# Performance work log

Measured on AMD Instinct MI355X. Metric: run time of the kernel, lower is better.

The kernel has to match this reference:

```python
import jax, jax.numpy as jnp
import numpy as np

B, L, HID = 1, 4096, 2048
H, P, N, CH, K = 64, 64, 128, 256, 4
INTER = H * P              # 4096 = num_heads * head_dim
CONV_DIM = INTER + 2 * N   # 4352
OUT_IN = 2 * (INTER + N) + H  # 8512, d_mlp == 0
DT_MIN, DT_MAX, EPS = 0.0, 100.0, 1e-5


def setup_inputs() -> dict:
    key = jax.random.key(0)
    ks = jax.random.split(key, 6)
    hidden_states = jax.random.normal(ks[0], (B, L, HID), jnp.float32)
    W_in = jax.random.normal(ks[1], (HID, OUT_IN), jnp.float32) * 0.02
    conv_w = jax.random.normal(ks[2], (K, CONV_DIM), jnp.float32) * 0.1
    conv_b = jnp.zeros((CONV_DIM,), jnp.float32)
    # dt_bias = softplus^{-1}(dt), dt ~ LogUniform[1e-3, 1e-1] (matches init_dt_bias)
    u = jax.random.uniform(ks[3], (H,))
    dt = jnp.exp(u * (jnp.log(0.1) - jnp.log(0.001)) + jnp.log(0.001))
    dt_bias = dt + jnp.log(-jnp.expm1(-dt))
    A_log = jnp.log(jax.random.uniform(ks[4], (H,), minval=1.0, maxval=16.0))
    D = jnp.ones((H,), jnp.float32)
    norm_weight = jnp.ones((INTER,), jnp.float32)
    W_out = jax.random.normal(ks[5], (INTER, HID), jnp.float32) * 0.02
    return dict(hidden_states=hidden_states, W_in=W_in, conv_w=conv_w, conv_b=conv_b,
                dt_bias=dt_bias, A_log=A_log, D=D, norm_weight=norm_weight, W_out=W_out)


def reference(hidden_states, W_in, conv_w, conv_b, dt_bias, A_log, D, norm_weight, W_out):
    Bsz, Ls, _ = hidden_states.shape
    nc = Ls // CH  # number of chunks

    zxbcdt = hidden_states @ W_in  # (b, l, 2*inter + 2*N + H); d_mlp = 0
    z, xBC, dt = jnp.split(zxbcdt, [INTER, 2 * INTER + 2 * N], axis=-1)

    # causal depthwise conv1d (left-pad K-1) + silu
    xp = jnp.pad(xBC, ((0, 0), (K - 1, 0), (0, 0)))
    xBC = sum(xp[:, k:k + Ls, :] * conv_w[k] for k in range(K)) + conv_b
    xBC = jax.nn.silu(xBC)
    x, Bt, Ct = jnp.split(xBC, [INTER, INTER + N], axis=-1)
    x = x.reshape(Bsz, Ls, H, P)

    dt = jnp.clip(jax.nn.softplus(dt + dt_bias), DT_MIN, DT_MAX)  # (b, l, h)
    A = -jnp.exp(A_log)  # (h,), negative

    # ---- chunked SSD (structured state-space duality) ----
    xc = x.reshape(Bsz, nc, CH, H, P)
    Bc = Bt.reshape(Bsz, nc, CH, N)   # shared across heads
    Cc = Ct.reshape(Bsz, nc, CH, N)
    dtc = dt.reshape(Bsz, nc, CH, H)
    xdt = xc * dtc[..., None]                     # discretized input
    dA = jnp.transpose(dtc * A, (0, 3, 1, 2))     # (b, h, c, l)
    A_cs = jnp.cumsum(dA, axis=-1)                # (b, h, c, l)

    # intra-chunk causal decay matrix L[i,j] = exp(sum_{j<k<=i} dA[k])
    seg = A_cs[..., :, None] - A_cs[..., None, :]
    tri = jnp.tril(jnp.ones((CH, CH), bool))
    Lmat = jnp.where(tri, jnp.exp(seg), 0.0)      # (b, h, c, l, s)
    Y_diag = jnp.einsum('bcln,bcsn,bhcls,bcshp->bclhp', Cc, Bc, Lmat, xdt)

    # per-chunk end states
    decay_states = jnp.exp(A_cs[..., -1:] - A_cs)  # (b, h, c, l)
    states = jnp.einsum('bcln,bhcl,bclhp->bchpn', Bc, decay_states, xdt)

    # inter-chunk recurrence via decay matrix over chunks (initial state = 0)
    chunk_end = A_cs[..., -1]                                     # (b, h, c)
    pad_cs = jnp.pad(jnp.cumsum(chunk_end, axis=-1), ((0, 0), (0, 0), (1, 0)))
    segc = pad_cs[..., :, None] - pad_cs[..., None, :]            # (b, h, c+1, c+1)
    tric = jnp.tril(jnp.ones((nc + 1, nc + 1), bool))
    decay_chunk = jnp.where(tric, jnp.exp(segc), 0.0)
    init = jnp.zeros((Bsz, 1, H, P, N), states.dtype)
    states = jnp.concatenate([init, states], axis=1)              # (b, c+1, h, p, n)
    new_states = jnp.einsum('bhzc,bchpn->bzhpn', decay_chunk, states)
    states_in = new_states[:, :-1]                                # state entering each chunk

    state_decay = jnp.exp(A_cs)  # (b, h, c, l)
    Y_off = jnp.einsum('bcln,bchpn,bhcl->bclhp', Cc, states_in, state_decay)

    y = (Y_diag + Y_off).reshape(Bsz, Ls, H, P)
    y = y + x * D[None, None, :, None]            # skip connection
    y = y.reshape(Bsz, Ls, INTER)

    # gated RMSNorm: rmsnorm(y * silu(z)) * weight  (fp32 internally)
    yf = y.astype(jnp.float32) * jax.nn.silu(z.astype(jnp.float32))
    var = jnp.mean(yf * yf, axis=-1, keepdims=True)
    yf = yf * jax.lax.rsqrt(var + EPS) * norm_weight
    y = yf.astype(hidden_states.dtype)

    return y @ W_out
```

## Files before the change

kernel.cpp:

```cpp
#include <hip/hip_runtime.h>
#include <hip/hip_bf16.h>
#include <math.h>

typedef __bf16 bf16x8 __attribute__((ext_vector_type(8)));
typedef float f32x4 __attribute__((ext_vector_type(4)));

#define GLOBAL_LOAD_LDS16(gptr, lptr) \
  __builtin_amdgcn_global_load_lds((const __attribute__((address_space(1))) void*)(gptr), \
                                   (__attribute__((address_space(3))) void*)(lptr), 16, 0, 0)

__device__ __forceinline__ void tile_map(int bid, int nbx, int nby, int& bx, int& by) {
  int nwg = nbx * nby;
  int q = nwg >> 3, r = nwg & 7;
  int xcd = bid & 7, orig = bid >> 3;
  int wgid = (xcd < r ? xcd * (q + 1) : r * (q + 1) + (xcd - r) * q) + orig;
  int per = nbx << 3;
  int grp = wgid / per;
  int rem = wgid - grp * per;
  int g0 = grp << 3;
  int gm = nby - g0; if (gm > 8) gm = 8;
  by = g0 + rem % gm;
  bx = rem / gm;
}

template<int MODE>
__global__ __launch_bounds__(256, 3)
void gemm_kernel(const __bf16* __restrict__ A, const __bf16* __restrict__ BT,
                 int M, int N, int K, int Ktot,
                 __bf16* __restrict__ out0, float* __restrict__ out2,
                 __bf16* yio, float* __restrict__ ssum,
                 const float* __restrict__ nwp)
{
  __shared__ __align__(16) __bf16 As[128 * 64];
  __shared__ __align__(16) __bf16 Bs[128 * 64];
  const int tid  = threadIdx.x;
  const int wave = tid >> 6, lane = tid & 63;
  const int quad = lane >> 4, l16 = lane & 15;
  int bx, by;
  tile_map(blockIdx.y * gridDim.x + blockIdx.x, gridDim.x, gridDim.y, bx, by);
  const int mBase = by * 128;
  const int nBase = bx * 128;
  const int wm = (wave & 1) * 64;
  const int wn = (wave >> 1) * 64;
  const int kb = (MODE == 3) ? blockIdx.z : 0;
  const int kStart = kb * K, kEnd = kb * K + K;

  f32x4 acc[4][4] = {};

  for (int k0 = kStart; k0 < kEnd; k0 += 64) {
    __syncthreads();
    for (int rd = 0; rd < 4; ++rd) {
      int p = rd * 256 + tid;
      int row = p >> 3;
      int lc  = (p & 7) ^ (row & 7);
      const __bf16* gpA = A + (size_t)(mBase + row) * Ktot + k0 + lc * 8;
      GLOBAL_LOAD_LDS16(gpA, As + rd * 2048 + wave * 512);
      int gr = nBase + row; if (gr >= N) gr = N - 1;
      const __bf16* gpB = BT + (size_t)gr * Ktot + k0 + lc * 8;
      GLOBAL_LOAD_LDS16(gpB, Bs + rd * 2048 + wave * 512);
    }
    __syncthreads();
#pragma unroll
    for (int ks = 0; ks < 2; ++ks) {
      bf16x8 af[4], bfr[4];
#pragma unroll
      for (int i = 0; i < 4; ++i) {
        int r = wm + i * 16 + l16;
        af[i]  = *(const bf16x8*)(As + (r << 6) + (((ks * 4 + quad) ^ (r & 7)) << 3));
        int rb = wn + i * 16 + l16;
        bfr[i] = *(const bf16x8*)(Bs + (rb << 6) + (((ks * 4 + quad) ^ (rb & 7)) << 3));
      }
#pragma unroll
      for (int i = 0; i < 4; ++i)
#pragma unroll
        for (int j = 0; j < 4; ++j)
          acc[i][j] = __builtin_amdgcn_mfma_f32_16x16x32_bf16(af[i], bfr[j], acc[i][j], 0, 0, 0);
    }
  }

  if (MODE == 2) {
    for (int i = 0; i < 4; ++i)
      for (int r = 0; r < 4; ++r) {
        int row = mBase + wm + i * 16 + quad * 4 + r;
        float sq = 0.f;
        for (int j = 0; j < 4; ++j) {
          int col = nBase + wn + j * 16 + l16;
          float v = acc[i][j][r];
          size_t idx = (size_t)row * 4096 + col;
          float y0 = (float)yio[idx];
          float zg = v / (1.f + expf(-v));
          float yf = y0 * zg;
          yio[idx] = (__bf16)(yf * nwp[col]);
          sq += yf * yf;
        }
        for (int m = 1; m < 16; m <<= 1) sq += __shfl_xor(sq, m, 64);
        if (l16 == 0) atomicAdd(&ssum[row], sq);
      }
  } else if (MODE == 3) {
    float rs[4][4];
    for (int i = 0; i < 4; ++i)
      for (int r = 0; r < 4; ++r) {
        int row = mBase + wm + i * 16 + quad * 4 + r;
        rs[i][r] = rsqrtf(ssum[row] / 4096.f + 1e-5f);
      }
    for (int i = 0; i < 4; ++i) {
      int rowl = wm + i * 16 + quad * 4;
      for (int j = 0; j < 4; ++j) {
        int col = nBase + wn + j * 16 + l16;
        for (int r = 0; r < 4; ++r) {
          int row = mBase + rowl + r;
          float o = acc[i][j][r] * rs[i][r];
          o = (o == o && fabsf(o) < 1e30f) ? o : 0.f;
          out2[(size_t)row * N + col] = o;
        }
      }
    }
  } else {
    for (int i = 0; i < 4; ++i) {
      int rowl = wm + i * 16 + quad * 4;
      for (int j = 0; j < 4; ++j) {
        int col = nBase + wn + j * 16 + l16;
        for (int r = 0; r < 4; ++r) {
          float v = acc[i][j][r];
          int row = mBase + rowl + r;
          if (col < 4352)       out0[(size_t)row * 4352 + col]        = (__bf16)v;
          else if (col < 4416)  out2[(size_t)row * 64 + (col - 4352)] = v;
        }
      }
    }
  }
}

__global__ __launch_bounds__(256)
void cast_kernel(const float* __restrict__ in, __bf16* __restrict__ out)
{
  size_t g = ((size_t)blockIdx.x * 256 + threadIdx.x) * 8;
  f32x4 a = *(const f32x4*)(in + g);
  f32x4 b = *(const f32x4*)(in + g + 4);
  bf16x8 v;
  for (int j = 0; j < 4; ++j) { v[j] = (__bf16)a[j]; v[4 + j] = (__bf16)b[j]; }
  *(bf16x8*)(out + g) = v;
}

__global__ __launch_bounds__(256)
void transpose_kernel(const float* __restrict__ in, __bf16* __restrict__ out,
                      int R, int C, int col0)
{
  __shared__ __bf16 tile[64][72];
  const int tid = threadIdx.x;
  const int r0 = blockIdx.y * 64, c0 = blockIdx.x * 64;
  const int tr = tid >> 3, tc = (tid & 7) * 8;
  for (int hh = 0; hh < 2; ++hh) {
    const float* gp = in + (size_t)(r0 + tr + hh * 32) * C + col0 + c0 + tc;
    f32x4 a = *(const f32x4*)gp;
    f32x4 b = *(const f32x4*)(gp + 4);
    for (int j = 0; j < 4; ++j) {
      tile[tr + hh * 32][tc + j]     = (__bf16)a[j];
      tile[tr + hh * 32][tc + 4 + j] = (__bf16)b[j];
    }
  }
  __syncthreads();
  for (int hh = 0; hh < 2; ++hh) {
    __bf16* op = out + (size_t)(c0 + tr + hh * 32) * R + r0 + tc;
    bf16x8 o;
    for (int j = 0; j < 8; ++j) o[j] = tile[tc + j][tr + hh * 32];
    *(bf16x8*)op = o;
  }
}

__global__ __launch_bounds__(256)
void conv_silu_kernel(const __bf16* __restrict__ xBCraw, const float* __restrict__ conv_w,
                      const float* __restrict__ conv_b,
                      __bf16* __restrict__ xconv, __bf16* __restrict__ Bmat,
                      __bf16* __restrict__ Cmat, __bf16* __restrict__ BTr)
{
  int g = blockIdx.x * 256 + threadIdx.x;
  int t = g / 544;
  int c = (g % 544) * 8;
  float acc[8];
  {
    f32x4 b0 = *(const f32x4*)(conv_b + c);
    f32x4 b1 = *(const f32x4*)(conv_b + c + 4);
    for (int j = 0; j < 4; ++j) { acc[j] = b0[j]; acc[4 + j] = b1[j]; }
  }
  for (int k = 0; k < 4; ++k) {
    int ts = t + k - 3;
    if (ts >= 0) {
      bf16x8 xv = *(const bf16x8*)(xBCraw + (size_t)ts * 4352 + c);
      f32x4 w0 = *(const f32x4*)(conv_w + (size_t)k * 4352 + c);
      f32x4 w1 = *(const f32x4*)(conv_w + (size_t)k * 4352 + c + 4);
      for (int j = 0; j < 4; ++j) {
        acc[j]     += (float)xv[j]     * w0[j];
        acc[4 + j] += (float)xv[4 + j] * w1[j];
      }
    }
  }
  for (int j = 0; j < 8; ++j) { float v = acc[j]; acc[j] = v / (1.f + expf(-v)); }
  bf16x8 o;
  for (int j = 0; j < 8; ++j) o[j] = (__bf16)acc[j];
  if (c < 4096) {
    *(bf16x8*)(xconv + (size_t)t * 4096 + c) = o;
  } else if (c < 4224) {
    int n = c - 4096;
    *(bf16x8*)(Bmat + (size_t)t * 128 + n) = o;
    for (int j = 0; j < 8; ++j) BTr[(size_t)(n + j) * 4096 + t] = o[j];
  } else {
    int n = c - 4224;
    *(bf16x8*)(Cmat + (size_t)t * 128 + n) = o;
  }
}

__global__ __launch_bounds__(256)
void dt_cumsum_kernel(const float* __restrict__ dtraw, const float* __restrict__ dt_bias,
                      const float* __restrict__ A_log, float* __restrict__ dtp,
                      float* __restrict__ csbuf)
{
  int h = blockIdx.x, cch = blockIdx.y, i = threadIdx.x;
  int t = cch * 256 + i;
  float x = dtraw[(size_t)t * 64 + h] + dt_bias[h];
  float sp = (x > 20.f) ? x : log1pf(expf(x));
  sp = fminf(fmaxf(sp, 0.f), 100.f);
  dtp[(size_t)t * 64 + h] = sp;
  float Ah = -expf(A_log[h]);
  __shared__ float s[256];
  s[i] = sp * Ah;
  __syncthreads();
  for (int off = 1; off < 256; off <<= 1) {
    float add = (i >= off) ? s[i - off] : 0.f;
    __syncthreads();
    s[i] += add;
    __syncthreads();
  }
  csbuf[(size_t)h * 4096 + t] = s[i];
}

__global__ __launch_bounds__(256)
void xdtT_kernel(const __bf16* __restrict__ xconv, const float* __restrict__ dtp,
                 __bf16* __restrict__ xdtT)
{
  __shared__ __bf16 tile[64][72];
  const int tid = threadIdx.x;
  const int t0 = blockIdx.y * 64, c0 = blockIdx.x * 64;
  const int tr = tid >> 3, tc = (tid & 7) * 8;
  const int h = (c0 + tc) >> 6;
  for (int hh = 0; hh < 2; ++hh) {
    int t = t0 + tr + hh * 32;
    float ds = dtp[(size_t)t * 64 + h];
    bf16x8 xv = *(const bf16x8*)(xconv + (size_t)t * 4096 + c0 + tc);
    for (int j = 0; j < 8; ++j) tile[tr + hh * 32][tc + j] = (__bf16)((float)xv[j] * ds);
  }
  __syncthreads();
  for (int hh = 0; hh < 2; ++hh) {
    __bf16* op = xdtT + (size_t)(c0 + tr + hh * 32) * 4096 + t0 + tc;
    bf16x8 o;
    for (int j = 0; j < 8; ++j) o[j] = tile[tc + j][tr + hh * 32];
    *(bf16x8*)op = o;
  }
}

__global__ __launch_bounds__(256)
void scores_kernel(const __bf16* __restrict__ Cmat, const __bf16* __restrict__ Bmat,
                   __bf16* __restrict__ scores)
{
  const int c = blockIdx.x;
  const int lb = blockIdx.y * 128, sb = blockIdx.z * 128;
  const int tid = threadIdx.x, wave = tid >> 6, lane = tid & 63;
  const int quad = lane >> 4, l16 = lane & 15;
  const int wl = (wave & 1) * 64, ws = (wave >> 1) * 64;
  f32x4 acc[4][4] = {};
  for (int k = 0; k < 4; ++k) {
    bf16x8 af[4], bfr[4];
    for (int i = 0; i < 4; ++i) {
      int tl = c * 256 + lb + wl + i * 16 + l16;
      af[i] = *(const bf16x8*)(Cmat + (size_t)tl * 128 + k * 32 + quad * 8);
    }
    for (int j = 0; j < 4; ++j) {
      int ts = c * 256 + sb + ws + j * 16 + l16;
      bfr[j] = *(const bf16x8*)(Bmat + (size_t)ts * 128 + k * 32 + quad * 8);
    }
    for (int i = 0; i < 4; ++i)
      for (int j = 0; j < 4; ++j)
        acc[i][j] = __builtin_amdgcn_mfma_f32_16x16x32_bf16(af[i], bfr[j], acc[i][j], 0, 0, 0);
  }
  for (int i = 0; i < 4; ++i)
    for (int j = 0; j < 4; ++j) {
      int lrow = lb + wl + i * 16 + quad * 4;
      int scol = sb + ws + j * 16 + l16;
      for (int r = 0; r < 4; ++r)
        scores[((size_t)c * 256 + lrow + r) * 256 + scol] = (__bf16)acc[i][j][r];
    }
}

__global__ __launch_bounds__(256)
void states_kernel(const __bf16* __restrict__ xdtT, const __bf16* __restrict__ BTr,
                   const float* __restrict__ csbuf, __bf16* __restrict__ chunk_states)
{
  const int c = blockIdx.x, h = blockIdx.y;
  const int tid = threadIdx.x, wave = tid >> 6, lane = tid & 63;
  const int quad = lane >> 4, l16 = lane & 15;
  __shared__ float decay[256];
  {
    float cs_end = csbuf[(size_t)h * 4096 + c * 256 + 255];
    decay[tid] = expf(fminf(cs_end - csbuf[(size_t)h * 4096 + c * 256 + tid], 0.f));
  }
  __syncthreads();
  const int wn = wave * 32;
  f32x4 acc[4][2] = {};
  for (int k = 0; k < 8; ++k) {
    bf16x8 af[4], bfr[2];
    for (int i = 0; i < 4; ++i) {
      int p = i * 16 + l16;
      af[i] = *(const bf16x8*)(xdtT + (size_t)(h * 64 + p) * 4096 + c * 256 + k * 32 + quad * 8);
    }
    for (int j = 0; j < 2; ++j) {
      int n = wn + j * 16 + l16;
      bf16x8 raw = *(const bf16x8*)(BTr + (size_t)n * 4096 + c * 256 + k * 32 + quad * 8);
      bf16x8 sc;
      for (int jj = 0; jj < 8; ++jj)
        sc[jj] = (__bf16)((float)raw[jj] * decay[k * 32 + quad * 8 + jj]);
      bfr[j] = sc;
    }
    for (int i = 0; i < 4; ++i)
      for (int j = 0; j < 2; ++j)
        acc[i][j] = __builtin_amdgcn_mfma_f32_16x16x32_bf16(af[i], bfr[j], acc[i][j], 0, 0, 0);
  }
  for (int i = 0; i < 4; ++i)
    for (int j = 0; j < 2; ++j) {
      int p = i * 16 + quad * 4;
      int n = wn + j * 16 + l16;
      for (int r = 0; r < 4; ++r)
        chunk_states[(((size_t)c * 64 + h) * 64 + p + r) * 128 + n] = (__bf16)acc[i][j][r];
    }
}

__global__ __launch_bounds__(256)
void scan_kernel(__bf16* states, const float* __restrict__ csbuf)
{
  size_t id = (size_t)blockIdx.x * 256 + threadIdx.x;
  int n = id & 127;
  int p = (int)((id >> 7) & 63);
  int h = (int)(id >> 13);
  float S = 0.f;
  for (int c = 0; c < 16; ++c) {
    size_t idx = (((size_t)c * 64 + h) * 64 + p) * 128 + n;
    float cst = (float)states[idx];
    states[idx] = (__bf16)S;
    float ce = csbuf[(size_t)h * 4096 + c * 256 + 255];
    S = S * expf(fminf(ce, 0.f)) + cst;
  }
}

__global__ __launch_bounds__(256)
void y_kernel(const __bf16* __restrict__ Cmat, const __bf16* __restrict__ states_in,
              const __bf16* __restrict__ scores, const __bf16* __restrict__ xdtT,
              const float* __restrict__ csbuf, const float* __restrict__ Dvec,
              __bf16* y)
{
  const int c = blockIdx.x, h = blockIdx.y;
  const int tid = threadIdx.x, wave = tid >> 6, lane = tid & 63;
  const int quad = lane >> 4, l16 = lane & 15;
  __shared__ float cs[256];
  cs[tid] = csbuf[(size_t)h * 4096 + c * 256 + tid];
  __syncthreads();
  const int wl = wave * 64;
  f32x4 acc[4][4] = {};

  for (int k = 0; k < 4; ++k) {
    bf16x8 af[4], bfr[4];
    for (int i = 0; i < 4; ++i) {
      int tl = c * 256 + wl + i * 16 + l16;
      af[i] = *(const bf16x8*)(Cmat + (size_t)tl * 128 + k * 32 + quad * 8);
    }
    for (int j = 0; j < 4; ++j) {
      int p = j * 16 + l16;
      bfr[j] = *(const bf16x8*)(states_in + (((size_t)c * 64 + h) * 64 + p) * 128 + k * 32 + quad * 8);
    }
    for (int i = 0; i < 4; ++i)
      for (int j = 0; j < 4; ++j)
        acc[i][j] = __builtin_amdgcn_mfma_f32_16x16x32_bf16(af[i], bfr[j], acc[i][j], 0, 0, 0);
  }
  for (int i = 0; i < 4; ++i)
    for (int r = 0; r < 4; ++r) {
      float sd = expf(fminf(cs[wl + i * 16 + quad * 4 + r], 0.f));
      for (int j = 0; j < 4; ++j) acc[i][j][r] *= sd;
    }
  for (int sb = 0; sb < 8; ++sb) {
    bf16x8 af[4], bfr[4];
    for (int i = 0; i < 4; ++i) {
      int lloc = wl + i * 16 + l16;
      bf16x8 raw = *(const bf16x8*)(scores + ((size_t)c * 256 + lloc) * 256 + sb * 32 + quad * 8);
      float csl = cs[lloc];
      bf16x8 w;
      for (int jj = 0; jj < 8; ++jj) {
        int s = sb * 32 + quad * 8 + jj;
        float e = expf(fminf(csl - cs[s], 0.f));
        float v = (s <= lloc) ? (float)raw[jj] * e : 0.f;
        w[jj] = (__bf16)v;
      }
      af[i] = w;
    }
    for (int j = 0; j < 4; ++j) {
      int p = j * 16 + l16;
      bfr[j] = *(const bf16x8*)(xdtT + (size_t)(h * 64 + p) * 4096 + c * 256 + sb * 32 + quad * 8);
    }
    for (int i = 0; i < 4; ++i)
      for (int j = 0; j < 4; ++j)
        acc[i][j] = __builtin_amdgcn_mfma_f32_16x16x32_bf16(af[i], bfr[j], acc[i][j], 0, 0, 0);
  }
  float Dh = Dvec[h];
  for (int i = 0; i < 4; ++i)
    for (int r = 0; r < 4; ++r) {
      int tl = c * 256 + wl + i * 16 + quad * 4 + r;
      for (int j = 0; j < 4; ++j) {
        int p = j * 16 + l16;
        size_t idx = (size_t)tl * 4096 + h * 64 + p;
        float xv = (float)y[idx];
        y[idx] = (__bf16)(acc[i][j][r] + xv * Dh);
      }
    }
}

extern "C" void kernel_launch(void* const* d_in, const int* in_sizes, int n_in,
                              void* d_out, int out_size, void* d_ws, size_t ws_size,
                              hipStream_t stream)
{
  const float* hs      = (const float*)d_in[0];
  const float* W_in    = (const float*)d_in[1];
  const float* conv_w  = (const float*)d_in[2];
  const float* conv_b  = (const float*)d_in[3];
  const float* dt_bias = (const float*)d_in[4];
  const float* A_log   = (const float*)d_in[5];
  const float* Dv      = (const float*)d_in[6];
  const float* nw      = (const float*)d_in[7];
  const float* W_out   = (const float*)d_in[8];
  float* out = (float*)d_out;

  char* base = (char*)d_ws;
  const size_t P0 = 0;
  const size_t P1 = 35651584;
  const size_t P2 = 69206016;
  const size_t P3 = 77611008;

  __bf16* xBCraw  = (__bf16*)(base + P0);
  __bf16* xdtT    = (__bf16*)(base + P0);
  __bf16* wTz     = (__bf16*)(base + P0);
  __bf16* wT_out  = (__bf16*)(base + P0);
  __bf16* wTa     = (__bf16*)(base + P1);
  __bf16* xconv   = (__bf16*)(base + P1);
  __bf16* Bmat    = (__bf16*)(base + P2);
  __bf16* Cmat    = (__bf16*)(base + P2 + 1048576);
  __bf16* BTr     = (__bf16*)(base + P2 + 2097152);
  float*  dtp     = (float*) (base + P2 + 3145728);
  float*  csbuf   = (float*) (base + P2 + 4194304);
  __bf16* scores  = (__bf16*)(base + P2 + 5242880);
  float*  dtraw   = (float*) (base + P2 + 7340032);
  float*  ssum    = (float*) (base + P2 + 8388608);
  __bf16* hs16    = (__bf16*)(base + P3);
  __bf16* states  = (__bf16*)d_out;

  hipMemsetAsync(ssum, 0, 4096 * sizeof(float), stream);
  cast_kernel<<<4096, 256, 0, stream>>>(hs, hs16);
  transpose_kernel<<<dim3(69, 32), 256, 0, stream>>>(W_in, wTa, 2048, 8512, 4096);
  gemm_kernel<0><<<dim3(35, 32), 256, 0, stream>>>(hs16, wTa, 4096, 4416, 2048, 2048,
                                                   xBCraw, dtraw, nullptr, nullptr, nullptr);
  conv_silu_kernel<<<8704, 256, 0, stream>>>(xBCraw, conv_w, conv_b, xconv, Bmat, Cmat, BTr);
  dt_cumsum_kernel<<<dim3(64, 16), 256, 0, stream>>>(dtraw, dt_bias, A_log, dtp, csbuf);
  xdtT_kernel<<<dim3(64, 64), 256, 0, stream>>>(xconv, dtp, xdtT);
  scores_kernel<<<dim3(16, 2, 2), 256, 0, stream>>>(Cmat, Bmat, scores);
  states_kernel<<<dim3(16, 64), 256, 0, stream>>>(xdtT, BTr, csbuf, states);
  scan_kernel<<<2048, 256, 0, stream>>>(states, csbuf);
  y_kernel<<<dim3(16, 64), 256, 0, stream>>>(Cmat, states, scores, xdtT, csbuf, Dv, xconv);
  transpose_kernel<<<dim3(64, 32), 256, 0, stream>>>(W_in, wTz, 2048, 8512, 0);
  gemm_kernel<2><<<dim3(32, 32), 256, 0, stream>>>(hs16, wTz, 4096, 4096, 2048, 2048,
                                                   nullptr, nullptr, xconv, ssum, nw);
  transpose_kernel<<<dim3(32, 64), 256, 0, stream>>>(W_out, wT_out, 4096, 2048, 0);
  gemm_kernel<3><<<dim3(16, 32, 1), 256, 0, stream>>>(xconv, wT_out, 4096, 2048, 4096, 4096,
                                                      nullptr, out, nullptr, ssum, nullptr);
}
```

Measured before the change: 582.7 us.

## Fuse conv, dt-scaling and transposes; add BK=128 z-gate GEMM kernel

Merges the conv+SiLU kernel with the separate xdt transpose kernel. The new kernel computes the conv per 64x64 tile, scales by dt and writes the transposed xdtT and BTr through shared memory. This removes a full re-read of xconv and the scattered per-element BTr stores. The z-gate GEMM moves to a dedicated kernel with a K-tile of 128, doubling LDS per block and lowering occupancy to 2, in exchange for fewer barriers. Workspace buffers are reshuffled (states into workspace, xdtT into the output buffer) to fit the new lifetimes.

```diff
diff --git a/kernel.cpp b/kernel.cpp
--- a/kernel.cpp
+++ b/kernel.cpp
@@ -28,8 +28,7 @@
 void gemm_kernel(const __bf16* __restrict__ A, const __bf16* __restrict__ BT,
                  int M, int N, int K, int Ktot,
                  __bf16* __restrict__ out0, float* __restrict__ out2,
-                 __bf16* yio, float* __restrict__ ssum,
-                 const float* __restrict__ nwp)
+                 float* __restrict__ ssum)
 {
   __shared__ __align__(16) __bf16 As[128 * 64];
   __shared__ __align__(16) __bf16 Bs[128 * 64];
@@ -42,12 +41,10 @@
   const int nBase = bx * 128;
   const int wm = (wave & 1) * 64;
   const int wn = (wave >> 1) * 64;
-  const int kb = (MODE == 3) ? blockIdx.z : 0;
-  const int kStart = kb * K, kEnd = kb * K + K;
 
   f32x4 acc[4][4] = {};
 
-  for (int k0 = kStart; k0 < kEnd; k0 += 64) {
+  for (int k0 = 0; k0 < K; k0 += 64) {
     __syncthreads();
     for (int rd = 0; rd < 4; ++rd) {
       int p = rd * 256 + tid;
@@ -78,25 +75,7 @@
     }
   }
 
-  if (MODE == 2) {
-    for (int i = 0; i < 4; ++i)
-      for (int r = 0; r < 4; ++r) {
-        int row = mBase + wm + i * 16 + quad * 4 + r;
-        float sq = 0.f;
-        for (int j = 0; j < 4; ++j) {
-          int col = nBase + wn + j * 16 + l16;
-          float v = acc[i][j][r];
-          size_t idx = (size_t)row * 4096 + col;
-          float y0 = (float)yio[idx];
-          float zg = v / (1.f + expf(-v));
-          float yf = y0 * zg;
-          yio[idx] = (__bf16)(yf * nwp[col]);
-          sq += yf * yf;
-        }
-        for (int m = 1; m < 16; m <<= 1) sq += __shfl_xor(sq, m, 64);
-        if (l16 == 0) atomicAdd(&ssum[row], sq);
-      }
-  } else if (MODE == 3) {
+  if (MODE == 3) {
     float rs[4][4];
     for (int i = 0; i < 4; ++i)
       for (int r = 0; r < 4; ++r) {
@@ -131,6 +110,74 @@
   }
 }
 
+__global__ __launch_bounds__(256, 2)
+void gemm128_z_kernel(const __bf16* __restrict__ A, const __bf16* __restrict__ BT,
+                      int Ktot, __bf16* yio, float* __restrict__ ssum,
+                      const float* __restrict__ nwp)
+{
+  __shared__ __align__(16) __bf16 As[128 * 128];
+  __shared__ __align__(16) __bf16 Bs[128 * 128];
+  const int tid  = threadIdx.x;
+  const int wave = tid >> 6, lane = tid & 63;
+  const int quad = lane >> 4, l16 = lane & 15;
+  int bx, by;
+  tile_map(blockIdx.y * gridDim.x + blockIdx.x, gridDim.x, gridDim.y, bx, by);
+  const int mBase = by * 128;
+  const int nBase = bx * 128;
+  const int wm = (wave & 1) * 64;
+  const int wn = (wave >> 1) * 64;
+
+  f32x4 acc[4][4] = {};
+
+  for (int k0 = 0; k0 < Ktot; k0 += 128) {
+    __syncthreads();
+    for (int rd = 0; rd < 8; ++rd) {
+      int p = rd * 256 + tid;
+      int row = p >> 4;
+      int lc  = (p & 15) ^ (row & 15);
+      const __bf16* gpA = A + (size_t)(mBase + row) * Ktot + k0 + lc * 8;
+      GLOBAL_LOAD_LDS16(gpA, As + rd * 2048 + wave * 512);
+      const __bf16* gpB = BT + (size_t)(nBase + row) * Ktot + k0 + lc * 8;
+      GLOBAL_LOAD_LDS16(gpB, Bs + rd * 2048 + wave * 512);
+    }
+    __syncthreads();
+#pragma unroll
+    for (int ks = 0; ks < 4; ++ks) {
+      bf16x8 af[4], bfr[4];
+#pragma unroll
+      for (int i = 0; i < 4; ++i) {
+        int r = wm + i * 16 + l16;
+        af[i]  = *(const bf16x8*)(As + (r << 7) + (((ks * 4 + quad) ^ (r & 15)) << 3));
+        int rb = wn + i * 16 + l16;
+        bfr[i] = *(const bf16x8*)(Bs + (rb << 7) + (((ks * 4 + quad) ^ (rb & 15)) << 3));
+      }
+#pragma unroll
+      for (int i = 0; i < 4; ++i)
+#pragma unroll
+        for (int j = 0; j < 4; ++j)
+          acc[i][j] = __builtin_amdgcn_mfma_f32_16x16x32_bf16(af[i], bfr[j], acc[i][j], 0, 0, 0);
+    }
+  }
+
+  for (int i = 0; i < 4; ++i)
+    for (int r = 0; r < 4; ++r) {
+      int row = mBase + wm + i * 16 + quad * 4 + r;
+      float sq = 0.f;
+      for (int j = 0; j < 4; ++j) {
+        int col = nBase + wn + j * 16 + l16;
+        float v = acc[i][j][r];
+        size_t idx = (size_t)row * 4096 + col;
+        float y0 = (float)yio[idx];
+        float zg = v / (1.f + expf(-v));
+        float yf = y0 * zg;
+        yio[idx] = (__bf16)(yf * nwp[col]);
+        sq += yf * yf;
+      }
+      for (int m = 1; m < 16; m <<= 1) sq += __shfl_xor(sq, m, 64);
+      if (l16 == 0) atomicAdd(&ssum[row], sq);
+    }
+}
+
 __global__ __launch_bounds__(256)
 void cast_kernel(const float* __restrict__ in, __bf16* __restrict__ out)
 {
@@ -169,44 +216,71 @@
 }
 
 __global__ __launch_bounds__(256)
-void conv_silu_kernel(const __bf16* __restrict__ xBCraw, const float* __restrict__ conv_w,
-                      const float* __restrict__ conv_b,
-                      __bf16* __restrict__ xconv, __bf16* __restrict__ Bmat,
-                      __bf16* __restrict__ Cmat, __bf16* __restrict__ BTr)
-{
-  int g = blockIdx.x * 256 + threadIdx.x;
-  int t = g / 544;
-  int c = (g % 544) * 8;
-  float acc[8];
+void conv_fused_kernel(const __bf16* __restrict__ xBCraw, const float* __restrict__ conv_w,
+                       const float* __restrict__ conv_b, const float* __restrict__ dtp,
+                       __bf16* __restrict__ xconv, __bf16* __restrict__ xdtT,
+                       __bf16* __restrict__ Bmat, __bf16* __restrict__ Cmat,
+                       __bf16* __restrict__ BTr)
+{
+  __shared__ __bf16 tile[64][72];
+  const int bx = blockIdx.x;
+  const int t0 = blockIdx.y * 64;
+  const int tid = threadIdx.x;
+  const int tr = tid >> 3, tc = (tid & 7) * 8;
+  const int cc = bx * 64 + tc;
+
+  float wgt[4][8], bias[8];
   {
-    f32x4 b0 = *(const f32x4*)(conv_b + c);
-    f32x4 b1 = *(const f32x4*)(conv_b + c + 4);
-    for (int j = 0; j < 4; ++j) { acc[j] = b0[j]; acc[4 + j] = b1[j]; }
-  }
-  for (int k = 0; k < 4; ++k) {
-    int ts = t + k - 3;
-    if (ts >= 0) {
-      bf16x8 xv = *(const bf16x8*)(xBCraw + (size_t)ts * 4352 + c);
-      f32x4 w0 = *(const f32x4*)(conv_w + (size_t)k * 4352 + c);
-      f32x4 w1 = *(const f32x4*)(conv_w + (size_t)k * 4352 + c + 4);
-      for (int j = 0; j < 4; ++j) {
-        acc[j]     += (float)xv[j]     * w0[j];
-        acc[4 + j] += (float)xv[4 + j] * w1[j];
-      }
-    }
-  }
-  for (int j = 0; j < 8; ++j) { float v = acc[j]; acc[j] = v / (1.f + expf(-v)); }
-  bf16x8 o;
-  for (int j = 0; j < 8; ++j) o[j] = (__bf16)acc[j];
-  if (c < 4096) {
-    *(bf16x8*)(xconv + (size_t)t * 4096 + c) = o;
-  } else if (c < 4224) {
-    int n = c - 4096;
-    *(bf16x8*)(Bmat + (size_t)t * 128 + n) = o;
-    for (int j = 0; j < 8; ++j) BTr[(size_t)(n + j) * 4096 + t] = o[j];
-  } else {
-    int n = c - 4224;
-    *(bf16x8*)(Cmat + (size_t)t * 128 + n) = o;
+    f32x4 b0 = *(const f32x4*)(conv_b + cc);
+    f32x4 b1 = *(const f32x4*)(conv_b + cc + 4);
+    for (int j = 0; j < 4; ++j) { bias[j] = b0[j]; bias[4 + j] = b1[j]; }
+    for (int k = 0; k < 4; ++k) {
+      f32x4 w0 = *(const f32x4*)(conv_w + (size_t)k * 4352 + cc);
+      f32x4 w1 = *(const f32x4*)(conv_w + (size_t)k * 4352 + cc + 4);
+      for (int j = 0; j < 4; ++j) { wgt[k][j] = w0[j]; wgt[k][4 + j] = w1[j]; }
+    }
+  }
+
+  for (int hh = 0; hh < 2; ++hh) {
+    int t = t0 + tr + hh * 32;
+    float acc[8];
+    for (int j = 0; j < 8; ++j) acc[j] = bias[j];
+    for (int k = 0; k < 4; ++k) {
+      int ts = t + k - 3;
+      if (ts >= 0) {
+        bf16x8 xv = *(const bf16x8*)(xBCraw + (size_t)ts * 4352 + cc);
+        for (int j = 0; j < 8; ++j) acc[j] += (float)xv[j] * wgt[k][j];
+      }
+    }
+    for (int j = 0; j < 8; ++j) { float v = acc[j]; acc[j] = v / (1.f + expf(-v)); }
+    bf16x8 o;
+    for (int j = 0; j < 8; ++j) o[j] = (__bf16)acc[j];
+    if (bx < 64) {
+      *(bf16x8*)(xconv + (size_t)t * 4096 + cc) = o;
+      float ds = dtp[(size_t)t * 64 + bx];
+      for (int j = 0; j < 8; ++j) tile[tr + hh * 32][tc + j] = (__bf16)(acc[j] * ds);
+    } else if (bx < 66) {
+      *(bf16x8*)(Bmat + (size_t)t * 128 + (cc - 4096)) = o;
+      for (int j = 0; j < 8; ++j) tile[tr + hh * 32][tc + j] = o[j];
+    } else {
+      *(bf16x8*)(Cmat + (size_t)t * 128 + (cc - 4224)) = o;
+    }
+  }
+  __syncthreads();
+  if (bx < 64) {
+    for (int hh = 0; hh < 2; ++hh) {
+      __bf16* op = xdtT + (size_t)(bx * 64 + tr + hh * 32) * 4096 + t0 + tc;
+      bf16x8 o;
+      for (int j = 0; j < 8; ++j) o[j] = tile[tc + j][tr + hh * 32];
+      *(bf16x8*)op = o;
+    }
+  } else if (bx < 66) {
+    for (int hh = 0; hh < 2; ++hh) {
+      __bf16* op = BTr + (size_t)((bx - 64) * 64 + tr + hh * 32) * 4096 + t0 + tc;
+      bf16x8 o;
+      for (int j = 0; j < 8; ++j) o[j] = tile[tc + j][tr + hh * 32];
+      *(bf16x8*)op = o;
+    }
   }
 }
 
@@ -235,30 +309,6 @@
 }
 
 __global__ __launch_bounds__(256)
-void xdtT_kernel(const __bf16* __restrict__ xconv, const float* __restrict__ dtp,
-                 __bf16* __restrict__ xdtT)
-{
-  __shared__ __bf16 tile[64][72];
-  const int tid = threadIdx.x;
-  const int t0 = blockIdx.y * 64, c0 = blockIdx.x * 64;
-  const int tr = tid >> 3, tc = (tid & 7) * 8;
-  const int h = (c0 + tc) >> 6;
-  for (int hh = 0; hh < 2; ++hh) {
-    int t = t0 + tr + hh * 32;
-    float ds = dtp[(size_t)t * 64 + h];
-    bf16x8 xv = *(const bf16x8*)(xconv + (size_t)t * 4096 + c0 + tc);
-    for (int j = 0; j < 8; ++j) tile[tr + hh * 32][tc + j] = (__bf16)((float)xv[j] * ds);
-  }
-  __syncthreads();
-  for (int hh = 0; hh < 2; ++hh) {
-    __bf16* op = xdtT + (size_t)(c0 + tr + hh * 32) * 4096 + t0 + tc;
-    bf16x8 o;
-    for (int j = 0; j < 8; ++j) o[j] = tile[tc + j][tr + hh * 32];
-    *(bf16x8*)op = o;
-  }
-}
-
-__global__ __launch_bounds__(256)
 void scores_kernel(const __bf16* __restrict__ Cmat, const __bf16* __restrict__ Bmat,
                    __bf16* __restrict__ scores)
 {
@@ -442,9 +492,9 @@
   const size_t P3 = 77611008;
 
   __bf16* xBCraw  = (__bf16*)(base + P0);
-  __bf16* xdtT    = (__bf16*)(base + P0);
+  __bf16* states  = (__bf16*)(base + P0);
   __bf16* wTz     = (__bf16*)(base + P0);
-  __bf16* wT_out  = (__bf16*)(base + P0);
+  __bf16* wT_out  = (__bf16*)(base + P0 + 16777216);
   __bf16* wTa     = (__bf16*)(base + P1);
   __bf16* xconv   = (__bf16*)(base + P1);
   __bf16* Bmat    = (__bf16*)(base + P2);
@@ -456,24 +506,23 @@
   float*  dtraw   = (float*) (base + P2 + 7340032);
   float*  ssum    = (float*) (base + P2 + 8388608);
   __bf16* hs16    = (__bf16*)(base + P3);
-  __bf16* states  = (__bf16*)d_out;
+  __bf16* xdtT    = (__bf16*)d_out;
 
   hipMemsetAsync(ssum, 0, 4096 * sizeof(float), stream);
   cast_kernel<<<4096, 256, 0, stream>>>(hs, hs16);
   transpose_kernel<<<dim3(69, 32), 256, 0, stream>>>(W_in, wTa, 2048, 8512, 4096);
   gemm_kernel<0><<<dim3(35, 32), 256, 0, stream>>>(hs16, wTa, 4096, 4416, 2048, 2048,
-                                                   xBCraw, dtraw, nullptr, nullptr, nullptr);
-  conv_silu_kernel<<<8704, 256, 0, stream>>>(xBCraw, conv_w, conv_b, xconv, Bmat, Cmat, BTr);
+                                                   xBCraw, dtraw, nullptr);
   dt_cumsum_kernel<<<dim3(64, 16), 256, 0, stream>>>(dtraw, dt_bias, A_log, dtp, csbuf);
-  xdtT_kernel<<<dim3(64, 64), 256, 0, stream>>>(xconv, dtp, xdtT);
+  conv_fused_kernel<<<dim3(68, 64), 256, 0, stream>>>(xBCraw, conv_w, conv_b, dtp,
+                                                      xconv, xdtT, Bmat, Cmat, BTr);
   scores_kernel<<<dim3(16, 2, 2), 256, 0, stream>>>(Cmat, Bmat, scores);
   states_kernel<<<dim3(16, 64), 256, 0, stream>>>(xdtT, BTr, csbuf, states);
   scan_kernel<<<2048, 256, 0, stream>>>(states, csbuf);
   y_kernel<<<dim3(16, 64), 256, 0, stream>>>(Cmat, states, scores, xdtT, csbuf, Dv, xconv);
   transpose_kernel<<<dim3(64, 32), 256, 0, stream>>>(W_in, wTz, 2048, 8512, 0);
-  gemm_kernel<2><<<dim3(32, 32), 256, 0, stream>>>(hs16, wTz, 4096, 4096, 2048, 2048,
-                                                   nullptr, nullptr, xconv, ssum, nw);
+  gemm128_z_kernel<<<dim3(32, 32), 256, 0, stream>>>(hs16, wTz, 2048, xconv, ssum, nw);
   transpose_kernel<<<dim3(32, 64), 256, 0, stream>>>(W_out, wT_out, 4096, 2048, 0);
   gemm_kernel<3><<<dim3(16, 32, 1), 256, 0, stream>>>(xconv, wT_out, 4096, 2048, 4096, 4096,
-                                                      nullptr, out, nullptr, ssum, nullptr);
-}
+                                                      nullptr, out, ssum);
+}
```

Result: faster. 564.6 us (-3.1%).
